# Optimization experiments

Hardware: AMD Instinct MI355X
Metric: run time of the kernel (lower is better)

The kernel has to match this reference:

```python
import jax, jax.numpy as jnp
import numpy as np

K = 9          # neighbors
DIL = 1        # dilation
BN_EPS = 1e-5

def _bn(x, g, b, m, v):
    # inference batchnorm over channel (last) dim
    return (x - m) * (g * jax.lax.rsqrt(v + BN_EPS)) + b

def setup_inputs() -> dict:
    key = jax.random.key(0)
    ks = jax.random.split(key, 4)
    B, C, H, W = 8, 192, 56, 56
    Ch = 384
    s = 0.02
    return {
        'x': jax.random.normal(ks[0], (B, C, H, W), jnp.float32),
        'fc1_w': jax.random.normal(ks[1], (C, C), jnp.float32) * s,
        'fc1_b': jnp.zeros((C,), jnp.float32),
        'bn1_g': jnp.ones((C,), jnp.float32), 'bn1_b': jnp.zeros((C,), jnp.float32),
        'bn1_m': jnp.zeros((C,), jnp.float32), 'bn1_v': jnp.ones((C,), jnp.float32),
        'gc_w': jax.random.normal(ks[2], (Ch, 2 * C), jnp.float32) * s,
        'gc_b': jnp.zeros((Ch,), jnp.float32),
        'bn2_g': jnp.ones((Ch,), jnp.float32), 'bn2_b': jnp.zeros((Ch,), jnp.float32),
        'bn2_m': jnp.zeros((Ch,), jnp.float32), 'bn2_v': jnp.ones((Ch,), jnp.float32),
        'fc2_w': jax.random.normal(ks[3], (C, Ch), jnp.float32) * s,
        'fc2_b': jnp.zeros((C,), jnp.float32),
        'bn3_g': jnp.ones((C,), jnp.float32), 'bn3_b': jnp.zeros((C,), jnp.float32),
        'bn3_m': jnp.zeros((C,), jnp.float32), 'bn3_v': jnp.ones((C,), jnp.float32),
    }

def reference(x, fc1_w, fc1_b, bn1_g, bn1_b, bn1_m, bn1_v,
              gc_w, gc_b, bn2_g, bn2_b, bn2_m, bn2_v,
              fc2_w, fc2_b, bn3_g, bn3_b, bn3_m, bn3_v):
    B, C, H, W = x.shape
    N = H * W
    xf = x.reshape(B, C, N).transpose(0, 2, 1)          # (B, N, C) nodes
    shortcut = xf
    # fc1: 1x1 conv + BN
    h = _bn(jnp.einsum('bnc,oc->bno', xf, fc1_w) + fc1_b, bn1_g, bn1_b, bn1_m, bn1_v)
    # dynamic KNN on L2-normalized features (ViG dense_knn_matrix)
    hn = h / jnp.maximum(jnp.linalg.norm(h, axis=-1, keepdims=True), 1e-12)
    sim = jnp.einsum('bnc,bmc->bnm', hn, hn)            # (B, N, N) cosine sim
    _, idx = jax.lax.top_k(sim, K * DIL)                # nearest (incl. self)
    idx = idx[..., ::DIL]                               # dilated neighbors (B,N,K)
    # gather neighbor features
    x_j = jax.vmap(lambda hb, ib: hb[ib])(h, idx)       # (B, N, K, C)
    x_i = h[:, :, None, :]                              # (B, N, 1, C)
    feat = jnp.concatenate([jnp.broadcast_to(x_i, x_j.shape), x_j - x_i], axis=-1)
    # EdgeConv: conv then max over neighbors
    e = jnp.einsum('bnke,oe->bnko', feat, gc_w) + gc_b  # (B, N, K, Ch)
    m = jnp.max(e, axis=2)                              # (B, N, Ch)
    m = jax.nn.gelu(_bn(m, bn2_g, bn2_b, bn2_m, bn2_v), approximate=False)
    # fc2: 1x1 conv + BN, residual
    out = _bn(jnp.einsum('bnh,oh->bno', m, fc2_w) + fc2_b, bn3_g, bn3_b, bn3_m, bn3_v)
    out = out + shortcut
    return out.transpose(0, 2, 1).reshape(B, C, H, W)
```

## Files before the change

kernel.cpp:

```cpp
#include <hip/hip_runtime.h>

#define BDIM 256
#define NB 8
#define NC 192
#define NN 3136
#define NCH 384
#define NK 9
#define NROW (NB * NN)

typedef __attribute__((ext_vector_type(8))) short short8;
typedef __attribute__((ext_vector_type(4))) float f32x4;

__device__ __forceinline__ unsigned short f2bf(float f) {
  union { float f; unsigned u; } x{f};
  unsigned r = x.u + 0x7fff + ((x.u >> 16) & 1);
  return (unsigned short)(r >> 16);
}

__device__ __forceinline__ float bf2f(unsigned u16) {
  union { unsigned u; float f; } x{u16 << 16};
  return x.f;
}

__device__ __forceinline__ unsigned fsort(float f) {
  union { float f; unsigned u; } x{f};
  return x.u ^ ((unsigned)(((int)x.u) >> 31) | 0x80000000u);
}

__device__ __forceinline__ void stage_tile(const char* gbase, char* lbuf, int t) {
#pragma unroll
  for (int i = 0; i < 6; ++i) {
    int L = (i * 256 + t) * 16;
    int m = L / 384;
    int kb = L - m * 384;
    const char* g = gbase + m * 384 + (kb ^ ((m & 7) << 4));
    __builtin_amdgcn_global_load_lds(
        (const __attribute__((address_space(1))) unsigned int*)g,
        (__attribute__((address_space(3))) unsigned int*)(lbuf + L), 16, 0, 0);
  }
}

__device__ __forceinline__ void stage_tile32(const char* gbase, char* lbuf, int t) {
#pragma unroll
  for (int i = 0; i < 3; ++i) {
    int L = (i * 256 + t) * 16;
    int m = L / 384;
    int kb = L - m * 384;
    const char* g = gbase + m * 384 + (kb ^ ((m & 7) << 4));
    __builtin_amdgcn_global_load_lds(
        (const __attribute__((address_space(1))) unsigned int*)g,
        (__attribute__((address_space(3))) unsigned int*)(lbuf + L), 16, 0, 0);
  }
}

__global__ __launch_bounds__(BDIM) void k0_convw(
    const float* __restrict__ gw, const float* __restrict__ f1w,
    const float* __restrict__ f2w, unsigned short* __restrict__ gcwb,
    unsigned short* __restrict__ fc1b, unsigned short* __restrict__ fc2b) {
  int i = (blockIdx.x * BDIM + threadIdx.x) * 4;
  const float* src;
  unsigned short* dst;
  if (i < 147456) {
    int o = i / NC, k = i - o * NC;
    src = gw + (size_t)(o < NCH ? o : o - NCH) * (2 * NC) + (o < NCH ? 0 : NC) + k;
    dst = gcwb + i;
  } else if (i < 184320) {
    int j = i - 147456;
    src = f1w + j;
    dst = fc1b + j;
  } else {
    int j = i - 184320;
    int o = j / NCH, k = j - o * NCH;
    int oc = o >> 6, om = o & 63;
    int kh = k / 192, km = k - kh * 192;
    src = f2w + j;
    dst = fc2b + ((size_t)((oc * 2 + kh) * 64 + om)) * 192 + km;
  }
  float4 v = *(const float4*)src;
  uint2 u;
  u.x = (unsigned)f2bf(v.x) | ((unsigned)f2bf(v.y) << 16);
  u.y = (unsigned)f2bf(v.z) | ((unsigned)f2bf(v.w) << 16);
  *(uint2*)dst = u;
}

__global__ __launch_bounds__(384) void k0b_params(
    const float* __restrict__ f1b, const float* __restrict__ g1,
    const float* __restrict__ b1, const float* __restrict__ m1,
    const float* __restrict__ v1, const float* __restrict__ gcb,
    const float* __restrict__ g2, const float* __restrict__ b2,
    const float* __restrict__ m2, const float* __restrict__ v2,
    const float* __restrict__ f2b, const float* __restrict__ g3,
    const float* __restrict__ b3, const float* __restrict__ m3,
    const float* __restrict__ v3, float* __restrict__ sc1,
    float* __restrict__ sh1, float* __restrict__ sc2, float* __restrict__ sh2,
    float* __restrict__ sc3, float* __restrict__ sh3) {
  int c = threadIdx.x;
  if (c < NC) {
    float s1 = g1[c] * rsqrtf(v1[c] + 1e-5f);
    sc1[c] = s1;
    sh1[c] = (f1b[c] - m1[c]) * s1 + b1[c];
    float s3 = g3[c] * rsqrtf(v3[c] + 1e-5f);
    sc3[c] = s3;
    sh3[c] = (f2b[c] - m3[c]) * s3 + b3[c];
  }
  float s2 = g2[c] * rsqrtf(v2[c] + 1e-5f);
  sc2[c] = s2;
  sh2[c] = (gcb[c] - m2[c]) * s2 + b2[c];
}

__global__ __launch_bounds__(BDIM) void k1_mfma(
    const float* __restrict__ x, const unsigned short* __restrict__ fc1b,
    const float* __restrict__ sc1, const float* __restrict__ sh1,
    unsigned short* __restrict__ hnb, float* __restrict__ normo) {
  __shared__ __align__(16) char abuf[2][24576];
  int t = threadIdx.x;
  int b = blockIdx.x / 49, n0 = (blockIdx.x % 49) * 64;
  int lane = t & 63, w = t >> 6;
  int l15 = lane & 15, l4 = lane >> 4;
  int n = n0 + w * 16 + l15;
  short8 bfr[6];
  {
    const float* xcol = x + (size_t)b * NC * NN + n;
#pragma unroll
    for (int ks = 0; ks < 6; ++ks) {
      union { short8 s; unsigned u[4]; } pk;
#pragma unroll
      for (int j = 0; j < 4; ++j) {
        float v0 = xcol[(size_t)(ks * 32 + l4 * 8 + 2 * j) * NN];
        float v1 = xcol[(size_t)(ks * 32 + l4 * 8 + 2 * j + 1) * NN];
        pk.u[j] = (unsigned)f2bf(v0) | ((unsigned)f2bf(v1) << 16);
      }
      bfr[ks] = pk.s;
    }
  }
  f32x4 acc[3][4];
#pragma unroll
  for (int oc = 0; oc < 3; ++oc)
#pragma unroll
    for (int sub = 0; sub < 4; ++sub) acc[oc][sub] = {0.f, 0.f, 0.f, 0.f};

  const char* wB = (const char*)fc1b;
  stage_tile(wB, abuf[0], t);
  __syncthreads();
  for (int oc = 0; oc < 3; ++oc) {
    int cur = oc & 1;
    if (oc < 2) stage_tile(wB + (size_t)(oc + 1) * 24576, abuf[cur ^ 1], t);
#pragma unroll
    for (int sub = 0; sub < 4; ++sub) {
      int r_ = sub * 16 + l15;
      int rbase = r_ * 384, sw = (r_ & 7) << 4;
#pragma unroll
      for (int ks = 0; ks < 6; ++ks) {
        short8 af = *(const short8*)&abuf[cur][rbase + ((ks * 64 + l4 * 16) ^ sw)];
        acc[oc][sub] = __builtin_amdgcn_mfma_f32_16x16x32_bf16(af, bfr[ks],
                                                               acc[oc][sub], 0, 0, 0);
      }
    }
    __syncthreads();
  }
  float p = 0.f;
#pragma unroll
  for (int oc = 0; oc < 3; ++oc)
#pragma unroll
    for (int sub = 0; sub < 4; ++sub) {
      int c4 = oc * 64 + sub * 16 + l4 * 4;
      float s_[4], h_[4];
      *(float4*)s_ = *(const float4*)&sc1[c4];
      *(float4*)h_ = *(const float4*)&sh1[c4];
#pragma unroll
      for (int r = 0; r < 4; ++r) {
        float v = acc[oc][sub][r] * s_[r] + h_[r];
        acc[oc][sub][r] = v;
        p += v * v;
      }
    }
  p += __shfl_xor(p, 16);
  p += __shfl_xor(p, 32);
  float nr = fmaxf(sqrtf(p), 1e-12f);
  float iv = 1.f / nr;
  if (l4 == 0) normo[(size_t)b * NN + n] = nr;
#pragma unroll
  for (int oc = 0; oc < 3; ++oc)
#pragma unroll
    for (int sub = 0; sub < 4; ++sub) {
      uint2 u;
      u.x = (unsigned)f2bf(acc[oc][sub][0] * iv) |
            ((unsigned)f2bf(acc[oc][sub][1] * iv) << 16);
      u.y = (unsigned)f2bf(acc[oc][sub][2] * iv) |
            ((unsigned)f2bf(acc[oc][sub][3] * iv) << 16);
      *(uint2*)&hnb[(size_t)(b * NN + n) * NC + oc * 64 + sub * 16 + l4 * 4] = u;
    }
}

__global__ __launch_bounds__(BDIM) void k2a_topk(
    const unsigned short* __restrict__ hnb, unsigned* __restrict__ candK) {
  __shared__ __align__(16) char abuf[2][12288];
  int t = threadIdx.x;
  int bid = blockIdx.x;
  int b = bid & 7;
  int g = bid >> 3;
  int n0 = (g >> 2) * 64;
  int seg = g & 3;
  int mt0 = (98 * seg) / 4, mt1 = (98 * (seg + 1)) / 4;
  const unsigned short* hb = hnb + (size_t)b * NN * NC;
  const char* hbB = (const char*)hb;
  int lane = t & 63, w = t >> 6;
  int l15 = lane & 15, l4 = lane >> 4;

  short8 bfr[6];
  {
    const short8* brow = (const short8*)(hb + (size_t)(n0 + w * 16 + l15) * NC + l4 * 8);
#pragma unroll
    for (int ks = 0; ks < 6; ++ks) bfr[ks] = brow[ks * 4];
  }
  unsigned tk[NK];
#pragma unroll
  for (int r = 0; r < NK; ++r) tk[r] = 0u;

  stage_tile32(hbB + (size_t)mt0 * 12288, abuf[0], t);
  __syncthreads();
  int nt = mt1 - mt0;
  for (int ti = 0; ti < nt; ++ti) {
    int cur = ti & 1;
    if (ti + 1 < nt)
      stage_tile32(hbB + (size_t)(mt0 + ti + 1) * 12288, abuf[cur ^ 1], t);
    int mglob = (mt0 + ti) * 32;
#pragma unroll
    for (int sub = 0; sub < 2; ++sub) {
      int r_ = sub * 16 + l15;
      int rbase = r_ * 384, sw = (r_ & 7) << 4;
      short8 af[6];
#pragma unroll
      for (int ks = 0; ks < 6; ++ks)
        af[ks] = *(const short8*)&abuf[cur][rbase + ((ks * 64 + l4 * 16) ^ sw)];
      f32x4 acc = {0.f, 0.f, 0.f, 0.f};
#pragma unroll
      for (int ks = 0; ks < 6; ++ks)
        acc = __builtin_amdgcn_mfma_f32_16x16x32_bf16(af[ks], bfr[ks], acc, 0, 0, 0);
      int mknd = 4095 - (mglob + sub * 16 + l4 * 4);
#pragma unroll
      for (int r = 0; r < 4; ++r) {
        unsigned cur_k = (fsort(acc[r]) & 0xFFFFF000u) | (unsigned)(mknd - r);
#pragma unroll
        for (int j = 0; j < NK; ++j) {
          unsigned hi = tk[j] > cur_k ? tk[j] : cur_k;
          unsigned lo = tk[j] > cur_k ? cur_k : tk[j];
          tk[j] = hi;
          cur_k = lo;
        }
      }
    }
    __syncthreads();
  }
  unsigned* mkeys = (unsigned*)&abuf[0][0];
  int nl = w * 16 + l15;
#pragma unroll
  for (int r = 0; r < NK; ++r) mkeys[(nl * 4 + l4) * NK + r] = tk[r];
  __syncthreads();
  if (t < 64) {
    const unsigned* src = &mkeys[t * 4 * NK];
    unsigned best[NK];
#pragma unroll
    for (int r = 0; r < NK; ++r) best[r] = 0u;
    for (int s = 0; s < 36; ++s) {
      unsigned cur_k = src[s];
#pragma unroll
      for (int q = 0; q < NK; ++q) {
        unsigned hi = best[q] > cur_k ? best[q] : cur_k;
        unsigned lo = best[q] > cur_k ? cur_k : best[q];
        best[q] = hi;
        cur_k = lo;
      }
    }
    size_t row = (size_t)b * NN + n0 + t;
#pragma unroll
    for (int r = 0; r < NK; ++r) candK[(size_t)(seg * NK + r) * NROW + row] = best[r];
  }
}

__global__ __launch_bounds__(BDIM) void k2b_merge(const unsigned* __restrict__ candK,
                                                  int* __restrict__ idxo) {
  int row = blockIdx.x * BDIM + threadIdx.x;
  unsigned tk[NK];
#pragma unroll
  for (int r = 0; r < NK; ++r) tk[r] = 0u;
  for (int s = 0; s < 4 * NK; ++s) {
    unsigned cur = candK[(size_t)s * NROW + row];
#pragma unroll
    for (int j = 0; j < NK; ++j) {
      unsigned hi = tk[j] > cur ? tk[j] : cur;
      unsigned lo = tk[j] > cur ? cur : tk[j];
      tk[j] = hi;
      cur = lo;
    }
  }
#pragma unroll
  for (int r = 0; r < NK; ++r)
    idxo[(size_t)row * NK + r] = 4095 - (int)(tk[r] & 4095u);
}

__global__ __launch_bounds__(BDIM) void k3_pq_mfma(
    const unsigned short* __restrict__ hnb, const unsigned short* __restrict__ gcwb,
    const float* __restrict__ norm, unsigned short* __restrict__ P,
    unsigned short* __restrict__ Q) {
  __shared__ __align__(16) char abuf[2][24576];
  int t = threadIdx.x;
  int b = blockIdx.x / 98;
  int rem = blockIdx.x % 98;
  int n0 = (rem >> 1) * 64;
  int ch0 = (rem & 1) * 6;
  const unsigned short* hb = hnb + (size_t)b * NN * NC;
  int lane = t & 63, w = t >> 6;
  int l15 = lane & 15, l4 = lane >> 4;
  int n = n0 + w * 16 + l15;
  short8 bfr[6];
  {
    const short8* brow = (const short8*)(hb + (size_t)n * NC + l4 * 8);
#pragma unroll
    for (int ks = 0; ks < 6; ++ks) bfr[ks] = brow[ks * 4];
  }
  float nrm = norm[(size_t)b * NN + n];
  size_t orow = (size_t)b * NN + n;
  const char* wB = (const char*)gcwb;

  stage_tile(wB + (size_t)ch0 * 24576, abuf[0], t);
  __syncthreads();
  for (int ci = 0; ci < 6; ++ci) {
    int ch = ch0 + ci;
    int cur = ci & 1;
    if (ci < 5) stage_tile(wB + (size_t)(ch + 1) * 24576, abuf[cur ^ 1], t);
#pragma unroll
    for (int sub = 0; sub < 4; ++sub) {
      int mrow = sub * 16 + l15;
      int rbase = mrow * 384, sw = (mrow & 7) << 4;
      f32x4 acc = {0.f, 0.f, 0.f, 0.f};
#pragma unroll
      for (int ks = 0; ks < 6; ++ks) {
        short8 af = *(const short8*)&abuf[cur][rbase + ((ks * 64 + l4 * 16) ^ sw)];
        acc = __builtin_amdgcn_mfma_f32_16x16x32_bf16(af, bfr[ks], acc, 0, 0, 0);
      }
      int o = ch * 64 + sub * 16 + l4 * 4;
      f32x4 st = acc * nrm;
      unsigned short* dst = (o < NCH) ? P : Q;
      int oo = (o < NCH) ? o : o - NCH;
      uint2 u;
      u.x = (unsigned)f2bf(st[0]) | ((unsigned)f2bf(st[1]) << 16);
      u.y = (unsigned)f2bf(st[2]) | ((unsigned)f2bf(st[3]) << 16);
      *(uint2*)&dst[orow * NCH + oo] = u;
    }
    __syncthreads();
  }
}

__global__ __launch_bounds__(BDIM) void k4_gathermax(
    const unsigned short* __restrict__ P, const unsigned short* __restrict__ Q,
    const int* __restrict__ idx, const float* __restrict__ sc2,
    const float* __restrict__ sh2, unsigned short* __restrict__ mbh) {
  int t = threadIdx.x;
  int lane = t & 63, wv = t >> 6;
  int row = blockIdx.x * 4 + wv;
  int b = row / NN, n = row % NN;
  const int* ip = idx + (size_t)row * NK;
  int id[NK];
#pragma unroll
  for (int k = 0; k < NK; ++k) id[k] = ip[k];
  const unsigned short* Qb = Q + (size_t)b * NN * NCH;
  const unsigned short* Pr = P + (size_t)row * NCH;
  const unsigned short* Qr = Qb + (size_t)n * NCH;
#pragma unroll
  for (int j = 0; j < 3; ++j) {
    int o = j * 128 + lane * 2;
    float mx0 = -1e30f, mx1 = -1e30f;
#pragma unroll
    for (int k = 0; k < NK; ++k) {
      unsigned g = *(const unsigned*)&Qb[(size_t)id[k] * NCH + o];
      mx0 = fmaxf(mx0, bf2f(g & 0xffffu));
      mx1 = fmaxf(mx1, bf2f(g >> 16));
    }
    unsigned pv = *(const unsigned*)&Pr[o];
    unsigned qv = *(const unsigned*)&Qr[o];
    float2 ss = *(const float2*)&sc2[o];
    float2 hh = *(const float2*)&sh2[o];
    float e0 = bf2f(pv & 0xffffu) - bf2f(qv & 0xffffu) + mx0;
    float e1 = bf2f(pv >> 16) - bf2f(qv >> 16) + mx1;
    float y0 = e0 * ss.x + hh.x;
    float y1 = e1 * ss.y + hh.y;
    float ge0 = 0.5f * y0 * (1.f + erff(y0 * 0.70710678118654752f));
    float ge1 = 0.5f * y1 * (1.f + erff(y1 * 0.70710678118654752f));
    *(unsigned*)&mbh[(size_t)row * NCH + o] =
        (unsigned)f2bf(ge0) | ((unsigned)f2bf(ge1) << 16);
  }
}

__global__ __launch_bounds__(BDIM) void k5_mfma(
    const unsigned short* __restrict__ mbh, const unsigned short* __restrict__ fc2b,
    const float* __restrict__ sc3, const float* __restrict__ sh3,
    const float* __restrict__ x, float* __restrict__ out) {
  __shared__ __align__(16) char abuf[2][24576];
  int t = threadIdx.x;
  int bid = blockIdx.x;
  int b = bid / 147;
  int rem = bid % 147;
  int n0 = (rem / 3) * 64;
  int oc = rem % 3;
  int lane = t & 63, w = t >> 6;
  int l15 = lane & 15, l4 = lane >> 4;
  int n = n0 + w * 16 + l15;
  short8 bfr[12];
  {
    const short8* brow = (const short8*)(mbh + (size_t)(b * NN + n) * NCH + l4 * 8);
#pragma unroll
    for (int kh = 0; kh < 2; ++kh)
#pragma unroll
      for (int ks = 0; ks < 6; ++ks) bfr[kh * 6 + ks] = brow[kh * 24 + ks * 4];
  }
  f32x4 acc[4];
#pragma unroll
  for (int sub = 0; sub < 4; ++sub) acc[sub] = {0.f, 0.f, 0.f, 0.f};

  const char* wt = (const char*)fc2b + (size_t)oc * 2 * 24576;
  stage_tile(wt, abuf[0], t);
  __syncthreads();
  for (int kh = 0; kh < 2; ++kh) {
    if (kh == 0) stage_tile(wt + 24576, abuf[1], t);
#pragma unroll
    for (int sub = 0; sub < 4; ++sub) {
      int r_ = sub * 16 + l15;
      int rbase = r_ * 384, sw = (r_ & 7) << 4;
#pragma unroll
      for (int ks = 0; ks < 6; ++ks) {
        short8 af = *(const short8*)&abuf[kh][rbase + ((ks * 64 + l4 * 16) ^ sw)];
        acc[sub] = __builtin_amdgcn_mfma_f32_16x16x32_bf16(af, bfr[kh * 6 + ks],
                                                           acc[sub], 0, 0, 0);
      }
    }
    __syncthreads();
  }
  const float* xb_ = x + (size_t)b * NC * NN;
  float* ob = out + (size_t)b * NC * NN;
#pragma unroll
  for (int sub = 0; sub < 4; ++sub) {
    int c4 = oc * 64 + sub * 16 + l4 * 4;
    float s_[4], h_[4];
    *(float4*)s_ = *(const float4*)&sc3[c4];
    *(float4*)h_ = *(const float4*)&sh3[c4];
#pragma unroll
    for (int r = 0; r < 4; ++r) {
      size_t off = (size_t)(c4 + r) * NN + n;
      ob[off] = acc[sub][r] * s_[r] + h_[r] + xb_[off];
    }
  }
}

extern "C" void kernel_launch(void* const* d_in, const int* in_sizes, int n_in,
                              void* d_out, int out_size, void* d_ws, size_t ws_size,
                              hipStream_t stream) {
  const float* x = (const float*)d_in[0];
  const float* fc1_w = (const float*)d_in[1];
  const float* fc1_b = (const float*)d_in[2];
  const float* bn1_g = (const float*)d_in[3];
  const float* bn1_b = (const float*)d_in[4];
  const float* bn1_m = (const float*)d_in[5];
  const float* bn1_v = (const float*)d_in[6];
  const float* gc_w = (const float*)d_in[7];
  const float* gc_b = (const float*)d_in[8];
  const float* bn2_g = (const float*)d_in[9];
  const float* bn2_b = (const float*)d_in[10];
  const float* bn2_m = (const float*)d_in[11];
  const float* bn2_v = (const float*)d_in[12];
  const float* fc2_w = (const float*)d_in[13];
  const float* fc2_b = (const float*)d_in[14];
  const float* bn3_g = (const float*)d_in[15];
  const float* bn3_b = (const float*)d_in[16];
  const float* bn3_m = (const float*)d_in[17];
  const float* bn3_v = (const float*)d_in[18];

  size_t nrow = (size_t)NROW;
  size_t npq = (size_t)NB * NN * NCH;
  size_t nhb = (size_t)NB * NN * NC;
  unsigned short* Pb = (unsigned short*)d_ws;
  unsigned short* Qb = Pb + npq;
  unsigned short* mbh = Qb + npq;
  float* norm = (float*)(mbh + npq);
  int* idx = (int*)(norm + nrow);
  unsigned short* hnb = (unsigned short*)(idx + nrow * NK);
  unsigned short* gcwb = hnb + nhb;
  unsigned short* fc1b = gcwb + 768 * NC;
  unsigned short* fc2b = fc1b + NC * NC;
  unsigned* candK = (unsigned*)(fc2b + NC * NCH);
  float* sc1 = (float*)(candK + 4 * NK * nrow);
  float* sh1 = sc1 + NC;
  float* sc2 = sh1 + NC;
  float* sh2 = sc2 + NCH;
  float* sc3 = sh2 + NCH;
  float* sh3 = sc3 + NC;

  k0_convw<<<252, BDIM, 0, stream>>>(gc_w, fc1_w, fc2_w, gcwb, fc1b, fc2b);
  k0b_params<<<1, 384, 0, stream>>>(fc1_b, bn1_g, bn1_b, bn1_m, bn1_v, gc_b,
                                    bn2_g, bn2_b, bn2_m, bn2_v, fc2_b, bn3_g,
                                    bn3_b, bn3_m, bn3_v, sc1, sh1, sc2, sh2,
                                    sc3, sh3);
  k1_mfma<<<NB * 49, BDIM, 0, stream>>>(x, fc1b, sc1, sh1, hnb, norm);
  k2a_topk<<<NB * 196, BDIM, 0, stream>>>(hnb, candK);
  k2b_merge<<<NROW / BDIM, BDIM, 0, stream>>>(candK, idx);
  k3_pq_mfma<<<NB * 98, BDIM, 0, stream>>>(hnb, gcwb, norm, Pb, Qb);
  k4_gathermax<<<(NB * NN) / 4, BDIM, 0, stream>>>(Pb, Qb, idx, sc2, sh2, mbh);
  k5_mfma<<<NB * 147, BDIM, 0, stream>>>(mbh, fc2b, sc3, sh3, x, (float*)d_out);
}
```

Measured before the change: 176.0 us.

## Fuse top-k and P/Q projection kernels into one launch with role-split blocks

The KNN top-k candidate kernel and the P/Q EdgeConv projection kernel are merged into a single launch, with blocks assigned one of two roles by block index: two of every three blocks do top-k and one does the projection. Both depend only on the normalized features, so running them in one grid lets them execute concurrently and share the GPU instead of serializing two launches. The projection path now uses 32-row weight tiles with a 24KB LDS buffer, so both roles fit the same shared-memory footprint. The cost is a heterogeneous grid whose role balance and tail behaviour may be uneven.

Result: faster. 164.2 us (-6.7%).

```diff
diff --git a/kernel.cpp b/kernel.cpp
--- a/kernel.cpp
+++ b/kernel.cpp
@@ -192,89 +192,141 @@
     }
 }
 
-__global__ __launch_bounds__(BDIM) void k2a_topk(
-    const unsigned short* __restrict__ hnb, unsigned* __restrict__ candK) {
+__global__ __launch_bounds__(BDIM) void k23_fused(
+    const unsigned short* __restrict__ hnb, const float* __restrict__ norm,
+    const unsigned short* __restrict__ gcwb, unsigned* __restrict__ candK,
+    unsigned short* __restrict__ P, unsigned short* __restrict__ Q) {
   __shared__ __align__(16) char abuf[2][12288];
   int t = threadIdx.x;
   int bid = blockIdx.x;
   int b = bid & 7;
-  int g = bid >> 3;
-  int n0 = (g >> 2) * 64;
-  int seg = g & 3;
-  int mt0 = (98 * seg) / 4, mt1 = (98 * (seg + 1)) / 4;
-  const unsigned short* hb = hnb + (size_t)b * NN * NC;
-  const char* hbB = (const char*)hb;
+  int j = bid >> 3;
+  int role3 = j % 3;
   int lane = t & 63, w = t >> 6;
   int l15 = lane & 15, l4 = lane >> 4;
-
-  short8 bfr[6];
-  {
-    const short8* brow = (const short8*)(hb + (size_t)(n0 + w * 16 + l15) * NC + l4 * 8);
-#pragma unroll
-    for (int ks = 0; ks < 6; ++ks) bfr[ks] = brow[ks * 4];
-  }
-  unsigned tk[NK];
-#pragma unroll
-  for (int r = 0; r < NK; ++r) tk[r] = 0u;
-
-  stage_tile32(hbB + (size_t)mt0 * 12288, abuf[0], t);
-  __syncthreads();
-  int nt = mt1 - mt0;
-  for (int ti = 0; ti < nt; ++ti) {
-    int cur = ti & 1;
-    if (ti + 1 < nt)
-      stage_tile32(hbB + (size_t)(mt0 + ti + 1) * 12288, abuf[cur ^ 1], t);
-    int mglob = (mt0 + ti) * 32;
-#pragma unroll
-    for (int sub = 0; sub < 2; ++sub) {
-      int r_ = sub * 16 + l15;
-      int rbase = r_ * 384, sw = (r_ & 7) << 4;
-      short8 af[6];
-#pragma unroll
-      for (int ks = 0; ks < 6; ++ks)
-        af[ks] = *(const short8*)&abuf[cur][rbase + ((ks * 64 + l4 * 16) ^ sw)];
-      f32x4 acc = {0.f, 0.f, 0.f, 0.f};
-#pragma unroll
-      for (int ks = 0; ks < 6; ++ks)
-        acc = __builtin_amdgcn_mfma_f32_16x16x32_bf16(af[ks], bfr[ks], acc, 0, 0, 0);
-      int mknd = 4095 - (mglob + sub * 16 + l4 * 4);
-#pragma unroll
-      for (int r = 0; r < 4; ++r) {
-        unsigned cur_k = (fsort(acc[r]) & 0xFFFFF000u) | (unsigned)(mknd - r);
-#pragma unroll
-        for (int j = 0; j < NK; ++j) {
-          unsigned hi = tk[j] > cur_k ? tk[j] : cur_k;
-          unsigned lo = tk[j] > cur_k ? cur_k : tk[j];
-          tk[j] = hi;
+  const unsigned short* hb = hnb + (size_t)b * NN * NC;
+
+  if (role3 != 2) {
+    int idx2a = (j / 3) * 2 + role3;
+    int n0 = (idx2a >> 2) * 64;
+    int seg = idx2a & 3;
+    int mt0 = (98 * seg) / 4, mt1 = (98 * (seg + 1)) / 4;
+    const char* hbB = (const char*)hb;
+
+    short8 bfr[6];
+    {
+      const short8* brow =
+          (const short8*)(hb + (size_t)(n0 + w * 16 + l15) * NC + l4 * 8);
+#pragma unroll
+      for (int ks = 0; ks < 6; ++ks) bfr[ks] = brow[ks * 4];
+    }
+    unsigned tk[NK];
+#pragma unroll
+    for (int r = 0; r < NK; ++r) tk[r] = 0u;
+
+    stage_tile32(hbB + (size_t)mt0 * 12288, abuf[0], t);
+    __syncthreads();
+    int nt = mt1 - mt0;
+    for (int ti = 0; ti < nt; ++ti) {
+      int cur = ti & 1;
+      if (ti + 1 < nt)
+        stage_tile32(hbB + (size_t)(mt0 + ti + 1) * 12288, abuf[cur ^ 1], t);
+      int mglob = (mt0 + ti) * 32;
+#pragma unroll
+      for (int sub = 0; sub < 2; ++sub) {
+        int r_ = sub * 16 + l15;
+        int rbase = r_ * 384, sw = (r_ & 7) << 4;
+        short8 af[6];
+#pragma unroll
+        for (int ks = 0; ks < 6; ++ks)
+          af[ks] = *(const short8*)&abuf[cur][rbase + ((ks * 64 + l4 * 16) ^ sw)];
+        f32x4 acc = {0.f, 0.f, 0.f, 0.f};
+#pragma unroll
+        for (int ks = 0; ks < 6; ++ks)
+          acc = __builtin_amdgcn_mfma_f32_16x16x32_bf16(af[ks], bfr[ks], acc, 0, 0, 0);
+        int mknd = 4095 - (mglob + sub * 16 + l4 * 4);
+#pragma unroll
+        for (int r = 0; r < 4; ++r) {
+          unsigned cur_k = (fsort(acc[r]) & 0xFFFFF000u) | (unsigned)(mknd - r);
+#pragma unroll
+          for (int q = 0; q < NK; ++q) {
+            unsigned hi = tk[q] > cur_k ? tk[q] : cur_k;
+            unsigned lo = tk[q] > cur_k ? cur_k : tk[q];
+            tk[q] = hi;
+            cur_k = lo;
+          }
+        }
+      }
+      __syncthreads();
+    }
+    unsigned* mkeys = (unsigned*)&abuf[0][0];
+    int nl = w * 16 + l15;
+#pragma unroll
+    for (int r = 0; r < NK; ++r) mkeys[(nl * 4 + l4) * NK + r] = tk[r];
+    __syncthreads();
+    if (t < 64) {
+      const unsigned* src = &mkeys[t * 4 * NK];
+      unsigned best[NK];
+#pragma unroll
+      for (int r = 0; r < NK; ++r) best[r] = 0u;
+      for (int s = 0; s < 36; ++s) {
+        unsigned cur_k = src[s];
+#pragma unroll
+        for (int q = 0; q < NK; ++q) {
+          unsigned hi = best[q] > cur_k ? best[q] : cur_k;
+          unsigned lo = best[q] > cur_k ? cur_k : best[q];
+          best[q] = hi;
           cur_k = lo;
         }
       }
-    }
+      size_t row = (size_t)b * NN + n0 + t;
+#pragma unroll
+      for (int r = 0; r < NK; ++r)
+        candK[(size_t)(seg * NK + r) * NROW + row] = best[r];
+    }
+  } else {
+    int jj = j / 3;
+    int n0 = (jj >> 1) * 64;
+    int half = jj & 1;
+    int n = n0 + w * 16 + l15;
+    short8 bfr[6];
+    {
+      const short8* brow = (const short8*)(hb + (size_t)n * NC + l4 * 8);
+#pragma unroll
+      for (int ks = 0; ks < 6; ++ks) bfr[ks] = brow[ks * 4];
+    }
+    float nrm = norm[(size_t)b * NN + n];
+    size_t orow = (size_t)b * NN + n;
+    const char* wB = (const char*)gcwb;
+
+    int ch0 = half * 12;
+    stage_tile32(wB + (size_t)ch0 * 12288, abuf[0], t);
     __syncthreads();
-  }
-  unsigned* mkeys = (unsigned*)&abuf[0][0];
-  int nl = w * 16 + l15;
-#pragma unroll
-  for (int r = 0; r < NK; ++r) mkeys[(nl * 4 + l4) * NK + r] = tk[r];
-  __syncthreads();
-  if (t < 64) {
-    const unsigned* src = &mkeys[t * 4 * NK];
-    unsigned best[NK];
-#pragma unroll
-    for (int r = 0; r < NK; ++r) best[r] = 0u;
-    for (int s = 0; s < 36; ++s) {
-      unsigned cur_k = src[s];
-#pragma unroll
-      for (int q = 0; q < NK; ++q) {
-        unsigned hi = best[q] > cur_k ? best[q] : cur_k;
-        unsigned lo = best[q] > cur_k ? cur_k : best[q];
-        best[q] = hi;
-        cur_k = lo;
-      }
-    }
-    size_t row = (size_t)b * NN + n0 + t;
-#pragma unroll
-    for (int r = 0; r < NK; ++r) candK[(size_t)(seg * NK + r) * NROW + row] = best[r];
+    for (int ci = 0; ci < 12; ++ci) {
+      int ch = ch0 + ci;
+      int cur = ci & 1;
+      if (ci < 11) stage_tile32(wB + (size_t)(ch + 1) * 12288, abuf[cur ^ 1], t);
+#pragma unroll
+      for (int sub = 0; sub < 2; ++sub) {
+        int mrow = sub * 16 + l15;
+        int rbase = mrow * 384, sw = (mrow & 7) << 4;
+        f32x4 acc = {0.f, 0.f, 0.f, 0.f};
+#pragma unroll
+        for (int ks = 0; ks < 6; ++ks) {
+          short8 af = *(const short8*)&abuf[cur][rbase + ((ks * 64 + l4 * 16) ^ sw)];
+          acc = __builtin_amdgcn_mfma_f32_16x16x32_bf16(af, bfr[ks], acc, 0, 0, 0);
+        }
+        int o = ch * 32 + sub * 16 + l4 * 4;
+        f32x4 st = acc * nrm;
+        unsigned short* dst = (o < NCH) ? P : Q;
+        int oo = (o < NCH) ? o : o - NCH;
+        uint2 u;
+        u.x = (unsigned)f2bf(st[0]) | ((unsigned)f2bf(st[1]) << 16);
+        u.y = (unsigned)f2bf(st[2]) | ((unsigned)f2bf(st[3]) << 16);
+        *(uint2*)&dst[orow * NCH + oo] = u;
+      }
+      __syncthreads();
+    }
   }
 }
 
@@ -297,59 +349,6 @@
 #pragma unroll
   for (int r = 0; r < NK; ++r)
     idxo[(size_t)row * NK + r] = 4095 - (int)(tk[r] & 4095u);
-}
-
-__global__ __launch_bounds__(BDIM) void k3_pq_mfma(
-    const unsigned short* __restrict__ hnb, const unsigned short* __restrict__ gcwb,
-    const float* __restrict__ norm, unsigned short* __restrict__ P,
-    unsigned short* __restrict__ Q) {
-  __shared__ __align__(16) char abuf[2][24576];
-  int t = threadIdx.x;
-  int b = blockIdx.x / 98;
-  int rem = blockIdx.x % 98;
-  int n0 = (rem >> 1) * 64;
-  int ch0 = (rem & 1) * 6;
-  const unsigned short* hb = hnb + (size_t)b * NN * NC;
-  int lane = t & 63, w = t >> 6;
-  int l15 = lane & 15, l4 = lane >> 4;
-  int n = n0 + w * 16 + l15;
-  short8 bfr[6];
-  {
-    const short8* brow = (const short8*)(hb + (size_t)n * NC + l4 * 8);
-#pragma unroll
-    for (int ks = 0; ks < 6; ++ks) bfr[ks] = brow[ks * 4];
-  }
-  float nrm = norm[(size_t)b * NN + n];
-  size_t orow = (size_t)b * NN + n;
-  const char* wB = (const char*)gcwb;
-
-  stage_tile(wB + (size_t)ch0 * 24576, abuf[0], t);
-  __syncthreads();
-  for (int ci = 0; ci < 6; ++ci) {
-    int ch = ch0 + ci;
-    int cur = ci & 1;
-    if (ci < 5) stage_tile(wB + (size_t)(ch + 1) * 24576, abuf[cur ^ 1], t);
-#pragma unroll
-    for (int sub = 0; sub < 4; ++sub) {
-      int mrow = sub * 16 + l15;
-      int rbase = mrow * 384, sw = (mrow & 7) << 4;
-      f32x4 acc = {0.f, 0.f, 0.f, 0.f};
-#pragma unroll
-      for (int ks = 0; ks < 6; ++ks) {
-        short8 af = *(const short8*)&abuf[cur][rbase + ((ks * 64 + l4 * 16) ^ sw)];
-        acc = __builtin_amdgcn_mfma_f32_16x16x32_bf16(af, bfr[ks], acc, 0, 0, 0);
-      }
-      int o = ch * 64 + sub * 16 + l4 * 4;
-      f32x4 st = acc * nrm;
-      unsigned short* dst = (o < NCH) ? P : Q;
-      int oo = (o < NCH) ? o : o - NCH;
-      uint2 u;
-      u.x = (unsigned)f2bf(st[0]) | ((unsigned)f2bf(st[1]) << 16);
-      u.y = (unsigned)f2bf(st[2]) | ((unsigned)f2bf(st[3]) << 16);
-      *(uint2*)&dst[orow * NCH + oo] = u;
-    }
-    __syncthreads();
-  }
 }
 
 __global__ __launch_bounds__(BDIM) void k4_gathermax(
@@ -501,9 +500,8 @@
                                     bn3_b, bn3_m, bn3_v, sc1, sh1, sc2, sh2,
                                     sc3, sh3);
   k1_mfma<<<NB * 49, BDIM, 0, stream>>>(x, fc1b, sc1, sh1, hnb, norm);
-  k2a_topk<<<NB * 196, BDIM, 0, stream>>>(hnb, candK);
+  k23_fused<<<NB * 294, BDIM, 0, stream>>>(hnb, norm, gcwb, candK, Pb, Qb);
   k2b_merge<<<NROW / BDIM, BDIM, 0, stream>>>(candK, idx);
-  k3_pq_mfma<<<NB * 98, BDIM, 0, stream>>>(hnb, gcwb, norm, Pb, Qb);
   k4_gathermax<<<(NB * NN) / 4, BDIM, 0, stream>>>(Pb, Qb, idx, sc2, sh2, mbh);
   k5_mfma<<<NB * 147, BDIM, 0, stream>>>(mbh, fc2b, sc3, sh3, x, (float*)d_out);
 }
```
